# Optimization experiments

Hardware: AMD Instinct MI355X
Metric: run time of the kernel (lower is better)

## Reference

```python
import jax, jax.numpy as jnp
import numpy as np

GF_R = 49      # guided filter radius (hardcoded in module)
GF_EPS = 1.0   # guided filter eps (hardcoded in module)


def edge_pad(x, r):
    # replicate-pad last two dims by r
    return jnp.pad(x, ((0, 0), (0, 0), (r, r), (r, r)), mode='edge')


def boxfilter(x, r):
    # integral-image box filter via cumsum chains, same shape out
    p = edge_pad(x, r)
    c = jnp.cumsum(p, axis=3)
    d = c[:, :, :, 2 * r:] - c[:, :, :, :-2 * r]
    c2 = jnp.cumsum(d, axis=2)
    return c2[:, :, 2 * r:, :] - c2[:, :, :-2 * r, :]


def guided_filter(x, r=GF_R, eps=GF_EPS):
    N = boxfilter(jnp.ones_like(x), r)
    mean_x = boxfilter(x, r) / N
    mean_x2 = boxfilter(x * x, r) / N
    var_x = mean_x2 - mean_x * mean_x   # cov_xy == var_x in the original code
    A = var_x / (var_x + eps)
    bb = mean_x - A * mean_x
    A = boxfilter(A, r) / N
    bb = boxfilter(bb, r) / N
    return A * x + bb


def setup_inputs() -> dict:
    key = jax.random.key(0)
    ks = jax.random.split(key, 12)
    m, n, r = 2048, 4096, 4
    m3 = len(np.arange(m)[::3])  # 683
    return {
        'b': jax.random.normal(ks[0], (1, 1, m, n), jnp.float32),
        'b_negative': jax.random.normal(ks[1], (1, 1, m3, n), jnp.float32),
        'foreground_b': jax.random.uniform(ks[2], (1, 1, m, n), jnp.float32),
        'hX': jax.random.normal(ks[3], (1, 1, m * r, n), jnp.float32),
        'recon_old': jax.random.normal(ks[4], (1, 1, m, n), jnp.float32),
        'fusion_mask': jax.random.uniform(ks[5], (1, 1, m, n), jnp.float32),
        'b_old': jax.random.normal(ks[6], (1, 1, m, n), jnp.float32),
        'r': r,
        'w': jax.random.normal(ks[7], (m, n), jnp.float32),
        'decay_col': jax.random.normal(ks[8], (1, 1, m3, n), jnp.float32),
        'ww': jax.random.normal(ks[9], (m, n), jnp.float32),
    }


def reference(b, b_negative, foreground_b, hX, recon_old, fusion_mask, b_old, r, w, decay_col, ww):
    m, n = w.shape
    b = b * jax.nn.softplus(w)
    # cumsum over coarse rows then bilinear upsample to (m, n)
    decay = jnp.cumsum(b_negative * jax.nn.softplus(decay_col), axis=-2)
    decay = jax.image.resize(decay, (1, 1, m, n), method='linear')
    b = jnp.cumsum(b, axis=-2)
    b = b + decay * (1.0 - foreground_b)
    b_adpt = b * fusion_mask + b_old * (1.0 - fusion_mask)
    diff = guided_filter(hX[:, :, ::r, :] + b_adpt - recon_old)
    diff_adpt = jnp.clip(jnp.diff(diff, axis=-2, prepend=diff[:, :, 0:1, :]), 0.0, None)
    diff_adpt = diff_adpt * jax.nn.softplus(ww)
    diff_adpt = jnp.cumsum(diff_adpt, axis=-2)
    b_adpt = b_adpt - diff_adpt
    return (b_adpt, diff, diff_adpt, b)
```

## Files before the change

kernel.cpp:

```cpp
#include <hip/hip_runtime.h>
#include <cstdint>
#include <cstddef>

#define MR 2048
#define NC 4096
#define M3 683
#define SEG 64
#define HSEG 32
#define SEGD 22
#define H3D 32
#define VT 64
#define VTILES 32
#define NORM (1.0f/9604.0f)
#define SK(k) ((k)+((k)>>4))

__device__ __forceinline__ float sp(float v){
  return fmaxf(v, 0.0f) + log1pf(expf(-fabsf(v)));
}


__global__ void seg_sum_both(const float* __restrict__ bneg, const float* __restrict__ dcol,
                             const float* __restrict__ b, const float* __restrict__ w,
                             float* __restrict__ TD, float* __restrict__ Pd,
                             float* __restrict__ TB, float* __restrict__ Pb){
  int s = blockIdx.x;
  int j = blockIdx.y*blockDim.x + threadIdx.x;
  if(s < SEGD){
    int i0 = s*H3D, i1 = min(M3, i0+H3D);
    float acc = 0.f;
    int i = i0;
    for(; i+8<=i1; i+=8){
      float bv[8], dv[8];
      #pragma unroll
      for(int t=0;t<8;t++){ bv[t]=bneg[(i+t)*NC+j]; dv[t]=dcol[(i+t)*NC+j]; }
      #pragma unroll
      for(int t=0;t<8;t++){ float x=bv[t]*sp(dv[t]); TD[(i+t)*NC+j]=x; acc+=x; }
    }
    for(; i<i1; i++){ float x=bneg[i*NC+j]*sp(dcol[i*NC+j]); TD[i*NC+j]=x; acc+=x; }
    Pd[s*NC+j] = acc;
  } else {
    int sb = s - SEGD;
    int i0 = sb*HSEG;
    float acc=0.f;
    for(int g=0;g<HSEG;g+=8){
      float bv[8], wv[8];
      #pragma unroll
      for(int t=0;t<8;t++){ int i=i0+g+t; bv[t]=b[i*NC+j]; wv[t]=w[i*NC+j]; }
      #pragma unroll
      for(int t=0;t<8;t++){ int i=i0+g+t; float x=bv[t]*sp(wv[t]); TB[i*NC+j]=x; acc+=x; }
    }
    Pb[sb*NC+j]=acc;
  }
}


__global__ void scan_excl_both(float* __restrict__ Pd, float* __restrict__ Pb){
  int j = blockIdx.x*blockDim.x + threadIdx.x;
  {
    float run=0.f; int s=0;
    for(; s+8<=SEGD; s+=8){
      float v[8];
      #pragma unroll
      for(int t=0;t<8;t++) v[t]=Pd[(s+t)*NC+j];
      #pragma unroll
      for(int t=0;t<8;t++){ Pd[(s+t)*NC+j]=run; run+=v[t]; }
    }
    for(; s<SEGD; s++){ float t=Pd[s*NC+j]; Pd[s*NC+j]=run; run+=t; }
  }
  {
    float run=0.f;
    for(int s=0; s<SEG; s+=8){
      float v[8];
      #pragma unroll
      for(int t=0;t<8;t++) v[t]=Pb[(s+t)*NC+j];
      #pragma unroll
      for(int t=0;t<8;t++){ Pb[(s+t)*NC+j]=run; run+=v[t]; }
    }
  }
}

template<int SEGS>
__global__ void scan_excl_t(float* __restrict__ P){
  int j = blockIdx.x*blockDim.x + threadIdx.x;
  float run=0.f;
  int s=0;
  for(; s+8<=SEGS; s+=8){
    float v[8];
    #pragma unroll
    for(int t=0;t<8;t++) v[t]=P[(s+t)*NC+j];
    #pragma unroll
    for(int t=0;t<8;t++){ P[(s+t)*NC+j]=run; run+=v[t]; }
  }
  for(; s<SEGS; s++){ float t=P[s*NC+j]; P[s*NC+j]=run; run+=t; }
}

__global__ void decay_finalize(const float* __restrict__ TD,
                               const float* __restrict__ Pd, float* __restrict__ dc){
  int s=blockIdx.x;
  int j=blockIdx.y*blockDim.x+threadIdx.x;
  int i0=s*H3D, i1=min(M3,i0+H3D);
  float run = Pd[s*NC+j];
  int i=i0;
  for(; i+8<=i1; i+=8){
    float tv[8];
    #pragma unroll
    for(int t=0;t<8;t++) tv[t]=TD[(i+t)*NC+j];
    #pragma unroll
    for(int t=0;t<8;t++){ run+=tv[t]; dc[(i+t)*NC+j]=run; }
  }
  for(; i<i1; i++){ run += TD[i*NC+j]; dc[i*NC+j]=run; }
}

__global__ void phase1(const float* __restrict__ TB,
                       const float* __restrict__ Pb, const float* __restrict__ dc,
                       const float* __restrict__ fg, const float* __restrict__ fm,
                       const float* __restrict__ bold, const float* __restrict__ hX,
                       const float* __restrict__ recon,
                       float* __restrict__ out0, float* __restrict__ out3,
                       float* __restrict__ X){
  int s=blockIdx.x;
  int j=blockIdx.y*blockDim.x+threadIdx.x;
  int i0=s*HSEG;
  float run = Pb[s*NC+j];
  for(int g=0; g<HSEG; g+=8){
    float tb[8], fgv[8], fmv[8], bo[8], hx[8], rc[8], d0[8], d1[8], fw[8];
    #pragma unroll
    for(int t=0;t<8;t++){
      int i=i0+g+t;
      tb[t]=TB[i*NC+j];
      fgv[t]=fg[i*NC+j];
      fmv[t]=fm[i*NC+j];
      bo[t]=bold[i*NC+j];
      hx[t]=hX[(size_t)(4*i)*NC+j];
      rc[t]=recon[i*NC+j];
      float c = (i+0.5f)*(683.0f/2048.0f)-0.5f;
      float fl = floorf(c);
      fw[t] = c-fl;
      int a0=(int)fl, a1=a0+1;
      a0 = a0<0?0:(a0>M3-1?M3-1:a0);
      a1 = a1<0?0:(a1>M3-1?M3-1:a1);
      d0[t]=dc[a0*NC+j]; d1[t]=dc[a1*NC+j];
    }
    #pragma unroll
    for(int t=0;t<8;t++){
      int i=i0+g+t;
      run += tb[t];
      float d = (1.f-fw[t])*d0[t] + fw[t]*d1[t];
      float bf = run + d*(1.f - fgv[t]);
      out3[i*NC+j]=bf;
      float ba = bf*fmv[t] + bo[t]*(1.f-fmv[t]);
      out0[i*NC+j]=ba;
      X[i*NC+j] = hx[t] + ba - rc[t];
    }
  }
}


__global__ __launch_bounds__(256) void hbox_sq(const float* __restrict__ X,
                         float* __restrict__ H1, float* __restrict__ H2){
  __shared__ float C1[SK(NC)+1];
  __shared__ float C2[SK(NC)+1];
  __shared__ float w1[4];
  __shared__ float w2[4];
  int row=blockIdx.x, tid=threadIdx.x;
  int lane = tid & 63, wvid = tid >> 6;
  const float* xr = X + (size_t)row*NC;
  float v1[16], v2[16];
  int base=tid*16;
  float run1=0.f,run2=0.f;
  const float4* p4 = reinterpret_cast<const float4*>(xr+base);
  #pragma unroll
  for(int q=0;q<4;q++){
    float4 fq=p4[q];
    float e[4]={fq.x,fq.y,fq.z,fq.w};
    #pragma unroll
    for(int t=0;t<4;t++){
      run1+=e[t];      v1[q*4+t]=run1;
      run2+=e[t]*e[t]; v2[q*4+t]=run2;
    }
  }
  float s1=run1, s2=run2;
  #pragma unroll
  for(int off=1;off<64;off<<=1){
    float o1=__shfl_up(s1,off);
    float o2=__shfl_up(s2,off);
    if(lane>=off){ s1+=o1; s2+=o2; }
  }
  if(lane==63){ w1[wvid]=s1; w2[wvid]=s2; }
  __syncthreads();
  float b1=0.f,b2=0.f;
  #pragma unroll
  for(int q=0;q<4;q++) if(q<wvid){ b1+=w1[q]; b2+=w2[q]; }
  float ex1 = b1 + s1 - run1, ex2 = b2 + s2 - run2;
  if(tid==0){C1[SK(0)]=0.f;C2[SK(0)]=0.f;}
  #pragma unroll
  for(int e=0;e<16;e++){ int k=base+1+e; C1[SK(k)]=ex1+v1[e]; C2[SK(k)]=ex2+v2[e]; }
  __syncthreads();
  float first1=C1[SK(1)],  last1=C1[SK(NC)]-C1[SK(NC-1)];
  float first2=C2[SK(1)],  last2=C2[SK(NC)]-C2[SK(NC-1)];
  float* h1 = H1+(size_t)row*NC;
  float* h2 = H2+(size_t)row*NC;
  #pragma unroll
  for(int k=0;k<16;k++){
    int j=k*256+tid;
    int lo=j-48, hi=j+49;
    int li = lo<0?0:lo;
    int hc = hi>NC-1?NC-1:hi;
    float s1w=C1[SK(hc+1)]-C1[SK(li)];
    float s2w=C2[SK(hc+1)]-C2[SK(li)];
    if(lo<0){ s1w+=(float)(-lo)*first1; s2w+=(float)(-lo)*first2; }
    if(hi>NC-1){ s1w+=(float)(hi-(NC-1))*last1; s2w+=(float)(hi-(NC-1))*last2; }
    h1[j]=s1w; h2[j]=s2w;
  }
}

__global__ __launch_bounds__(256) void hbox_two(const float* __restrict__ A,
                         const float* __restrict__ B,
                         float* __restrict__ H1, float* __restrict__ H2){
  __shared__ float C1[SK(NC)+1];
  __shared__ float C2[SK(NC)+1];
  __shared__ float w1[4];
  __shared__ float w2[4];
  int row=blockIdx.x, tid=threadIdx.x;
  int lane = tid & 63, wvid = tid >> 6;
  const float* ar = A + (size_t)row*NC;
  const float* br = B + (size_t)row*NC;
  float v1[16], v2[16];
  int base=tid*16;
  float run1=0.f,run2=0.f;
  const float4* pa = reinterpret_cast<const float4*>(ar+base);
  const float4* pb = reinterpret_cast<const float4*>(br+base);
  #pragma unroll
  for(int q=0;q<4;q++){
    float4 fa=pa[q]; float4 fb=pb[q];
    float ea[4]={fa.x,fa.y,fa.z,fa.w};
    float eb[4]={fb.x,fb.y,fb.z,fb.w};
    #pragma unroll
    for(int t=0;t<4;t++){
      run1+=ea[t]; v1[q*4+t]=run1;
      run2+=eb[t]; v2[q*4+t]=run2;
    }
  }
  float s1=run1, s2=run2;
  #pragma unroll
  for(int off=1;off<64;off<<=1){
    float o1=__shfl_up(s1,off);
    float o2=__shfl_up(s2,off);
    if(lane>=off){ s1+=o1; s2+=o2; }
  }
  if(lane==63){ w1[wvid]=s1; w2[wvid]=s2; }
  __syncthreads();
  float b1=0.f,b2=0.f;
  #pragma unroll
  for(int q=0;q<4;q++) if(q<wvid){ b1+=w1[q]; b2+=w2[q]; }
  float ex1 = b1 + s1 - run1, ex2 = b2 + s2 - run2;
  if(tid==0){C1[SK(0)]=0.f;C2[SK(0)]=0.f;}
  #pragma unroll
  for(int e=0;e<16;e++){ int k=base+1+e; C1[SK(k)]=ex1+v1[e]; C2[SK(k)]=ex2+v2[e]; }
  __syncthreads();
  float first1=C1[SK(1)], last1=C1[SK(NC)]-C1[SK(NC-1)];
  float first2=C2[SK(1)], last2=C2[SK(NC)]-C2[SK(NC-1)];
  float* h1 = H1+(size_t)row*NC;
  float* h2 = H2+(size_t)row*NC;
  #pragma unroll
  for(int k=0;k<16;k++){
    int j=k*256+tid;
    int lo=j-48, hi=j+49;
    int li = lo<0?0:lo;
    int hc = hi>NC-1?NC-1:hi;
    float s1w=C1[SK(hc+1)]-C1[SK(li)];
    float s2w=C2[SK(hc+1)]-C2[SK(li)];
    if(lo<0){ s1w+=(float)(-lo)*first1; s2w+=(float)(-lo)*first2; }
    if(hi>NC-1){ s1w+=(float)(hi-(NC-1))*last1; s2w+=(float)(hi-(NC-1))*last2; }
    h1[j]=s1w; h2[j]=s2w;
  }
}


__global__ void vbox_stage1(const float* __restrict__ H1, const float* __restrict__ H2,
                            float* __restrict__ Aimg, float* __restrict__ BBimg){
  int tile = blockIdx.x;
  int j = blockIdx.y*blockDim.x + threadIdx.x;
  int i0 = tile*VT;
  int ip = i0-1;
  float Sa=0.f, Sb=0.f;
  for(int g=0; g<98; g+=14){
    float a1[14], a2[14];
    #pragma unroll
    for(int t=0;t<14;t++){
      int c = ip-48+g+t;
      int cc = c<0?0:(c>MR-1?MR-1:c);
      a1[t]=H1[cc*NC+j]; a2[t]=H2[cc*NC+j];
    }
    #pragma unroll
    for(int t=0;t<14;t++){ Sa+=a1[t]; Sb+=a2[t]; }
  }
  for(int g=0; g<VT; g+=8){
    float hu1[8],hd1[8],hu2[8],hd2[8];
    #pragma unroll
    for(int t=0;t<8;t++){
      int i=i0+g+t;
      int up=i+49; up=up>MR-1?MR-1:up;
      int dn=i-49; dn=dn<0?0:dn;
      hu1[t]=H1[up*NC+j]; hd1[t]=H1[dn*NC+j];
      hu2[t]=H2[up*NC+j]; hd2[t]=H2[dn*NC+j];
    }
    #pragma unroll
    for(int t=0;t<8;t++){
      int i=i0+g+t;
      Sa += hu1[t]-hd1[t];
      Sb += hu2[t]-hd2[t];
      float mx = Sa*NORM, mx2 = Sb*NORM;
      float var = mx2 - mx*mx;
      float A = var/(var+1.0f);
      float bb = mx - A*mx;
      Aimg[i*NC+j]=A; BBimg[i*NC+j]=bb;
    }
  }
}


__global__ void vbox2_fused(const float* __restrict__ H1, const float* __restrict__ H2,
                            const float* __restrict__ X, const float* __restrict__ ww,
                            float* __restrict__ diff, float* __restrict__ S,
                            float* __restrict__ Pc){
  int tile = blockIdx.x;
  int j = blockIdx.y*blockDim.x + threadIdx.x;
  int i0 = tile*VT;
  int ip = i0-1;
  float Sa=0.f, Sb=0.f;
  for(int g=0; g<98; g+=14){
    float a1[14], a2[14];
    #pragma unroll
    for(int t=0;t<14;t++){
      int c = ip-48+g+t;
      int cc = c<0?0:(c>MR-1?MR-1:c);
      a1[t]=H1[cc*NC+j]; a2[t]=H2[cc*NC+j];
    }
    #pragma unroll
    for(int t=0;t<14;t++){ Sa+=a1[t]; Sb+=a2[t]; }
  }
  float dpre, acc=0.f;
  if(tile==0) dpre = 3.0e38f;
  else        dpre = (Sa*NORM)*X[(size_t)ip*NC+j] + Sb*NORM;
  for(int g=0; g<VT; g+=8){
    float hu1[8],hd1[8],hu2[8],hd2[8],xv[8],wv[8];
    #pragma unroll
    for(int t=0;t<8;t++){
      int i=i0+g+t;
      int up=i+49; up=up>MR-1?MR-1:up;
      int dn=i-49; dn=dn<0?0:dn;
      hu1[t]=H1[up*NC+j]; hd1[t]=H1[dn*NC+j];
      hu2[t]=H2[up*NC+j]; hd2[t]=H2[dn*NC+j];
      xv[t]=X[(size_t)i*NC+j]; wv[t]=ww[i*NC+j];
    }
    #pragma unroll
    for(int t=0;t<8;t++){
      int i=i0+g+t;
      Sa += hu1[t]-hd1[t];
      Sb += hu2[t]-hd2[t];
      float d = (Sa*NORM)*xv[t] + Sb*NORM;
      diff[i*NC+j]=d;
      float v = d-dpre; v = v>0.f? v:0.f;
      float sv = v*sp(wv[t]);
      S[i*NC+j]=sv; acc+=sv; dpre=d;
    }
  }
  Pc[tile*NC+j]=acc;
}


__global__ void phase3_final(const float* __restrict__ Pc,
                             float* __restrict__ out0, float* __restrict__ out2){
  int s=blockIdx.x;
  int j=blockIdx.y*blockDim.x+threadIdx.x;
  int i0=s*VT;
  float run = Pc[s*NC+j];
  for(int g=0; g<VT; g+=8){
    float sv[8], o0[8];
    #pragma unroll
    for(int t=0;t<8;t++){ int i=i0+g+t; sv[t]=out2[i*NC+j]; o0[t]=out0[i*NC+j]; }
    #pragma unroll
    for(int t=0;t<8;t++){
      int i=i0+g+t;
      run += sv[t];
      out2[i*NC+j]=run;
      out0[i*NC+j]=o0[t]-run;
    }
  }
}

extern "C" void kernel_launch(void* const* d_in, const int* in_sizes, int n_in,
                              void* d_out, int out_size, void* d_ws, size_t ws_size,
                              hipStream_t stream){
  const float* b    = (const float*)d_in[0];
  const float* bneg = (const float*)d_in[1];
  const float* fg   = (const float*)d_in[2];
  const float* hX   = (const float*)d_in[3];
  const float* recon= (const float*)d_in[4];
  const float* fm   = (const float*)d_in[5];
  const float* bold = (const float*)d_in[6];
  const float* w    = (const float*)d_in[8];
  const float* dcol = (const float*)d_in[9];
  const float* ww   = (const float*)d_in[10];

  float* out  = (float*)d_out;
  float* out0 = out;
  float* out1 = out + (size_t)MR*NC;
  float* out2 = out + 2ull*MR*NC;
  float* out3 = out + 3ull*MR*NC;

  float* wsf = (float*)d_ws;
  float* X  = wsf;
  float* H1 = wsf + 1ull*MR*NC;
  float* H2 = wsf + 2ull*MR*NC;
  float* DC = wsf + 3ull*MR*NC;
  float* Pb = DC + (size_t)M3*NC;
  float* Pd = Pb + (size_t)SEG*NC;
  float* Pc = Pd + (size_t)SEGD*NC;
  float* TD = H1;
  float* TB = H2;

  seg_sum_both <<<dim3(SEGD+SEG,NC/256),256,0,stream>>>(bneg,dcol,b,w,TD,Pd,TB,Pb);
  scan_excl_both<<<NC/256,256,0,stream>>>(Pd,Pb);
  decay_finalize<<<dim3(SEGD,NC/256),256,0,stream>>>(TD,Pd,DC);
  phase1       <<<dim3(SEG, NC/256),256,0,stream>>>(TB,Pb,DC,fg,fm,bold,hX,recon,out0,out3,X);
  hbox_sq      <<<MR,256,0,stream>>>(X,H1,H2);
  vbox_stage1  <<<dim3(VTILES,NC/256),256,0,stream>>>(H1,H2,out1,out2);
  hbox_two     <<<MR,256,0,stream>>>(out1,out2,H1,H2);
  vbox2_fused  <<<dim3(VTILES,NC/256),256,0,stream>>>(H1,H2,X,ww,out1,out2,Pc);
  scan_excl_t<VTILES><<<NC/256,256,0,stream>>>(Pc);
  phase3_final <<<dim3(VTILES,NC/256),256,0,stream>>>(Pc,out0,out2);
}
```

Measured before the change: 569.2 us.

## Vectorize column kernels with float4/float2 accesses and split final scan finer

Column-parallel kernels now handle four (or two) adjacent columns per thread using float4/float2 loads and stores, and the grids shrink to match. The hbox kernels gather each thread's 16 contiguous outputs into registers and write them as float4 stores instead of strided scalar stores. vbox2_fused now emits two partial sums per tile so the final cumulative pass runs over 64 segments, keeping enough blocks in flight. The aim is fewer memory instructions and wider transactions. The cost is higher register pressure and fewer blocks in the wide kernels, which can reduce occupancy.

```diff
diff --git a/kernel.cpp b/kernel.cpp
--- a/kernel.cpp
+++ b/kernel.cpp
@@ -11,8 +11,12 @@
 #define H3D 32
 #define VT 64
 #define VTILES 32
+#define PSEG 64
 #define NORM (1.0f/9604.0f)
 #define SK(k) ((k)+((k)>>4))
+
+union F4u { float4 v; float f[4]; };
+union F2u { float2 v; float f[2]; };
 
 __device__ __forceinline__ float sp(float v){
   return fmaxf(v, 0.0f) + log1pf(expf(-fabsf(v)));
@@ -24,32 +28,52 @@
                              float* __restrict__ TD, float* __restrict__ Pd,
                              float* __restrict__ TB, float* __restrict__ Pb){
   int s = blockIdx.x;
-  int j = blockIdx.y*blockDim.x + threadIdx.x;
+  size_t col = ((size_t)blockIdx.y*blockDim.x + threadIdx.x)*4;
   if(s < SEGD){
     int i0 = s*H3D, i1 = min(M3, i0+H3D);
-    float acc = 0.f;
+    float acc[4]={0.f,0.f,0.f,0.f};
     int i = i0;
     for(; i+8<=i1; i+=8){
-      float bv[8], dv[8];
-      #pragma unroll
-      for(int t=0;t<8;t++){ bv[t]=bneg[(i+t)*NC+j]; dv[t]=dcol[(i+t)*NC+j]; }
-      #pragma unroll
-      for(int t=0;t<8;t++){ float x=bv[t]*sp(dv[t]); TD[(i+t)*NC+j]=x; acc+=x; }
-    }
-    for(; i<i1; i++){ float x=bneg[i*NC+j]*sp(dcol[i*NC+j]); TD[i*NC+j]=x; acc+=x; }
-    Pd[s*NC+j] = acc;
+      F4u bv[8], dv[8];
+      #pragma unroll
+      for(int t=0;t<8;t++){ size_t o=(size_t)(i+t)*NC+col;
+        bv[t].v=*(const float4*)(bneg+o); dv[t].v=*(const float4*)(dcol+o); }
+      #pragma unroll
+      for(int t=0;t<8;t++){
+        F4u x; size_t o=(size_t)(i+t)*NC+col;
+        #pragma unroll
+        for(int k=0;k<4;k++){ x.f[k]=bv[t].f[k]*sp(dv[t].f[k]); acc[k]+=x.f[k]; }
+        *(float4*)(TD+o)=x.v;
+      }
+    }
+    for(; i<i1; i++){
+      F4u bv,dv,x; size_t o=(size_t)i*NC+col;
+      bv.v=*(const float4*)(bneg+o); dv.v=*(const float4*)(dcol+o);
+      #pragma unroll
+      for(int k=0;k<4;k++){ x.f[k]=bv.f[k]*sp(dv.f[k]); acc[k]+=x.f[k]; }
+      *(float4*)(TD+o)=x.v;
+    }
+    F4u a; a.f[0]=acc[0];a.f[1]=acc[1];a.f[2]=acc[2];a.f[3]=acc[3];
+    *(float4*)(Pd+(size_t)s*NC+col)=a.v;
   } else {
     int sb = s - SEGD;
     int i0 = sb*HSEG;
-    float acc=0.f;
+    float acc[4]={0.f,0.f,0.f,0.f};
     for(int g=0;g<HSEG;g+=8){
-      float bv[8], wv[8];
-      #pragma unroll
-      for(int t=0;t<8;t++){ int i=i0+g+t; bv[t]=b[i*NC+j]; wv[t]=w[i*NC+j]; }
-      #pragma unroll
-      for(int t=0;t<8;t++){ int i=i0+g+t; float x=bv[t]*sp(wv[t]); TB[i*NC+j]=x; acc+=x; }
-    }
-    Pb[sb*NC+j]=acc;
+      F4u bv[8], wv[8];
+      #pragma unroll
+      for(int t=0;t<8;t++){ size_t o=(size_t)(i0+g+t)*NC+col;
+        bv[t].v=*(const float4*)(b+o); wv[t].v=*(const float4*)(w+o); }
+      #pragma unroll
+      for(int t=0;t<8;t++){
+        F4u x; size_t o=(size_t)(i0+g+t)*NC+col;
+        #pragma unroll
+        for(int k=0;k<4;k++){ x.f[k]=bv[t].f[k]*sp(wv[t].f[k]); acc[k]+=x.f[k]; }
+        *(float4*)(TB+o)=x.v;
+      }
+    }
+    F4u a; a.f[0]=acc[0];a.f[1]=acc[1];a.f[2]=acc[2];a.f[3]=acc[3];
+    *(float4*)(Pb+(size_t)sb*NC+col)=a.v;
   }
 }
 
@@ -97,18 +121,30 @@
 __global__ void decay_finalize(const float* __restrict__ TD,
                                const float* __restrict__ Pd, float* __restrict__ dc){
   int s=blockIdx.x;
-  int j=blockIdx.y*blockDim.x+threadIdx.x;
+  size_t col = ((size_t)blockIdx.y*blockDim.x + threadIdx.x)*4;
   int i0=s*H3D, i1=min(M3,i0+H3D);
-  float run = Pd[s*NC+j];
+  float run[4];
+  { F4u p; p.v=*(const float4*)(Pd+(size_t)s*NC+col);
+    run[0]=p.f[0];run[1]=p.f[1];run[2]=p.f[2];run[3]=p.f[3]; }
   int i=i0;
   for(; i+8<=i1; i+=8){
-    float tv[8];
-    #pragma unroll
-    for(int t=0;t<8;t++) tv[t]=TD[(i+t)*NC+j];
-    #pragma unroll
-    for(int t=0;t<8;t++){ run+=tv[t]; dc[(i+t)*NC+j]=run; }
-  }
-  for(; i<i1; i++){ run += TD[i*NC+j]; dc[i*NC+j]=run; }
+    F4u tv[8];
+    #pragma unroll
+    for(int t=0;t<8;t++) tv[t].v=*(const float4*)(TD+(size_t)(i+t)*NC+col);
+    #pragma unroll
+    for(int t=0;t<8;t++){
+      F4u o;
+      #pragma unroll
+      for(int k=0;k<4;k++){ run[k]+=tv[t].f[k]; o.f[k]=run[k]; }
+      *(float4*)(dc+(size_t)(i+t)*NC+col)=o.v;
+    }
+  }
+  for(; i<i1; i++){
+    F4u tv,o; tv.v=*(const float4*)(TD+(size_t)i*NC+col);
+    #pragma unroll
+    for(int k=0;k<4;k++){ run[k]+=tv.f[k]; o.f[k]=run[k]; }
+    *(float4*)(dc+(size_t)i*NC+col)=o.v;
+  }
 }
 
 __global__ void phase1(const float* __restrict__ TB,
@@ -119,38 +155,50 @@
                        float* __restrict__ out0, float* __restrict__ out3,
                        float* __restrict__ X){
   int s=blockIdx.x;
-  int j=blockIdx.y*blockDim.x+threadIdx.x;
+  size_t col = ((size_t)blockIdx.y*blockDim.x + threadIdx.x)*4;
   int i0=s*HSEG;
-  float run = Pb[s*NC+j];
-  for(int g=0; g<HSEG; g+=8){
-    float tb[8], fgv[8], fmv[8], bo[8], hx[8], rc[8], d0[8], d1[8], fw[8];
-    #pragma unroll
-    for(int t=0;t<8;t++){
+  float run[4];
+  { F4u p; p.v=*(const float4*)(Pb+(size_t)s*NC+col);
+    run[0]=p.f[0];run[1]=p.f[1];run[2]=p.f[2];run[3]=p.f[3]; }
+  for(int g=0; g<HSEG; g+=4){
+    F4u tb[4], fgv[4], fmv[4], bo[4], hx[4], rc[4], d0[4], d1[4];
+    float fw[4];
+    #pragma unroll
+    for(int t=0;t<4;t++){
       int i=i0+g+t;
-      tb[t]=TB[i*NC+j];
-      fgv[t]=fg[i*NC+j];
-      fmv[t]=fm[i*NC+j];
-      bo[t]=bold[i*NC+j];
-      hx[t]=hX[(size_t)(4*i)*NC+j];
-      rc[t]=recon[i*NC+j];
-      float c = (i+0.5f)*(683.0f/2048.0f)-0.5f;
-      float fl = floorf(c);
-      fw[t] = c-fl;
+      size_t o=(size_t)i*NC+col;
+      tb[t].v =*(const float4*)(TB+o);
+      fgv[t].v=*(const float4*)(fg+o);
+      fmv[t].v=*(const float4*)(fm+o);
+      bo[t].v =*(const float4*)(bold+o);
+      hx[t].v =*(const float4*)(hX+(size_t)(4*i)*NC+col);
+      rc[t].v =*(const float4*)(recon+o);
+      float c=(i+0.5f)*(683.0f/2048.0f)-0.5f;
+      float fl=floorf(c); fw[t]=c-fl;
       int a0=(int)fl, a1=a0+1;
-      a0 = a0<0?0:(a0>M3-1?M3-1:a0);
-      a1 = a1<0?0:(a1>M3-1?M3-1:a1);
-      d0[t]=dc[a0*NC+j]; d1[t]=dc[a1*NC+j];
-    }
-    #pragma unroll
-    for(int t=0;t<8;t++){
+      a0=a0<0?0:(a0>M3-1?M3-1:a0);
+      a1=a1<0?0:(a1>M3-1?M3-1:a1);
+      d0[t].v=*(const float4*)(dc+(size_t)a0*NC+col);
+      d1[t].v=*(const float4*)(dc+(size_t)a1*NC+col);
+    }
+    #pragma unroll
+    for(int t=0;t<4;t++){
       int i=i0+g+t;
-      run += tb[t];
-      float d = (1.f-fw[t])*d0[t] + fw[t]*d1[t];
-      float bf = run + d*(1.f - fgv[t]);
-      out3[i*NC+j]=bf;
-      float ba = bf*fmv[t] + bo[t]*(1.f-fmv[t]);
-      out0[i*NC+j]=ba;
-      X[i*NC+j] = hx[t] + ba - rc[t];
+      size_t o=(size_t)i*NC+col;
+      F4u o3v,o0v,xv;
+      #pragma unroll
+      for(int k=0;k<4;k++){
+        run[k]+=tb[t].f[k];
+        float d=(1.f-fw[t])*d0[t].f[k]+fw[t]*d1[t].f[k];
+        float bf=run[k]+d*(1.f-fgv[t].f[k]);
+        o3v.f[k]=bf;
+        float ba=bf*fmv[t].f[k]+bo[t].f[k]*(1.f-fmv[t].f[k]);
+        o0v.f[k]=ba;
+        xv.f[k]=hx[t].f[k]+ba-rc[t].f[k];
+      }
+      *(float4*)(out3+o)=o3v.v;
+      *(float4*)(out0+o)=o0v.v;
+      *(float4*)(X+o)=xv.v;
     }
   }
 }
@@ -200,9 +248,10 @@
   float first2=C2[SK(1)],  last2=C2[SK(NC)]-C2[SK(NC-1)];
   float* h1 = H1+(size_t)row*NC;
   float* h2 = H2+(size_t)row*NC;
-  #pragma unroll
-  for(int k=0;k<16;k++){
-    int j=k*256+tid;
+  F4u s1o[4], s2o[4];
+  #pragma unroll
+  for(int e=0;e<16;e++){
+    int j=base+e;
     int lo=j-48, hi=j+49;
     int li = lo<0?0:lo;
     int hc = hi>NC-1?NC-1:hi;
@@ -210,7 +259,12 @@
     float s2w=C2[SK(hc+1)]-C2[SK(li)];
     if(lo<0){ s1w+=(float)(-lo)*first1; s2w+=(float)(-lo)*first2; }
     if(hi>NC-1){ s1w+=(float)(hi-(NC-1))*last1; s2w+=(float)(hi-(NC-1))*last2; }
-    h1[j]=s1w; h2[j]=s2w;
+    s1o[e>>2].f[e&3]=s1w; s2o[e>>2].f[e&3]=s2w;
+  }
+  #pragma unroll
+  for(int q=0;q<4;q++){
+    *(float4*)(h1+base+4*q)=s1o[q].v;
+    *(float4*)(h2+base+4*q)=s2o[q].v;
   }
 }
 
@@ -262,9 +316,10 @@
   float first2=C2[SK(1)], last2=C2[SK(NC)]-C2[SK(NC-1)];
   float* h1 = H1+(size_t)row*NC;
   float* h2 = H2+(size_t)row*NC;
-  #pragma unroll
-  for(int k=0;k<16;k++){
-    int j=k*256+tid;
+  F4u s1o[4], s2o[4];
+  #pragma unroll
+  for(int e=0;e<16;e++){
+    int j=base+e;
     int lo=j-48, hi=j+49;
     int li = lo<0?0:lo;
     int hc = hi>NC-1?NC-1:hi;
@@ -272,7 +327,12 @@
     float s2w=C2[SK(hc+1)]-C2[SK(li)];
     if(lo<0){ s1w+=(float)(-lo)*first1; s2w+=(float)(-lo)*first2; }
     if(hi>NC-1){ s1w+=(float)(hi-(NC-1))*last1; s2w+=(float)(hi-(NC-1))*last2; }
-    h1[j]=s1w; h2[j]=s2w;
+    s1o[e>>2].f[e&3]=s1w; s2o[e>>2].f[e&3]=s2w;
+  }
+  #pragma unroll
+  for(int q=0;q<4;q++){
+    *(float4*)(h1+base+4*q)=s1o[q].v;
+    *(float4*)(h2+base+4*q)=s2o[q].v;
   }
 }
 
@@ -280,41 +340,52 @@
 __global__ void vbox_stage1(const float* __restrict__ H1, const float* __restrict__ H2,
                             float* __restrict__ Aimg, float* __restrict__ BBimg){
   int tile = blockIdx.x;
-  int j = blockIdx.y*blockDim.x + threadIdx.x;
+  size_t col = ((size_t)blockIdx.y*blockDim.x + threadIdx.x)*2;
   int i0 = tile*VT;
   int ip = i0-1;
-  float Sa=0.f, Sb=0.f;
+  float Sa[2]={0.f,0.f}, Sb[2]={0.f,0.f};
   for(int g=0; g<98; g+=14){
-    float a1[14], a2[14];
+    F2u a1[14], a2[14];
     #pragma unroll
     for(int t=0;t<14;t++){
       int c = ip-48+g+t;
       int cc = c<0?0:(c>MR-1?MR-1:c);
-      a1[t]=H1[cc*NC+j]; a2[t]=H2[cc*NC+j];
-    }
-    #pragma unroll
-    for(int t=0;t<14;t++){ Sa+=a1[t]; Sb+=a2[t]; }
+      a1[t].v=*(const float2*)(H1+(size_t)cc*NC+col);
+      a2[t].v=*(const float2*)(H2+(size_t)cc*NC+col);
+    }
+    #pragma unroll
+    for(int t=0;t<14;t++){
+      #pragma unroll
+      for(int k=0;k<2;k++){ Sa[k]+=a1[t].f[k]; Sb[k]+=a2[t].f[k]; }
+    }
   }
   for(int g=0; g<VT; g+=8){
-    float hu1[8],hd1[8],hu2[8],hd2[8];
+    F2u hu1[8],hd1[8],hu2[8],hd2[8];
     #pragma unroll
     for(int t=0;t<8;t++){
       int i=i0+g+t;
       int up=i+49; up=up>MR-1?MR-1:up;
       int dn=i-49; dn=dn<0?0:dn;
-      hu1[t]=H1[up*NC+j]; hd1[t]=H1[dn*NC+j];
-      hu2[t]=H2[up*NC+j]; hd2[t]=H2[dn*NC+j];
+      hu1[t].v=*(const float2*)(H1+(size_t)up*NC+col);
+      hd1[t].v=*(const float2*)(H1+(size_t)dn*NC+col);
+      hu2[t].v=*(const float2*)(H2+(size_t)up*NC+col);
+      hd2[t].v=*(const float2*)(H2+(size_t)dn*NC+col);
     }
     #pragma unroll
     for(int t=0;t<8;t++){
       int i=i0+g+t;
-      Sa += hu1[t]-hd1[t];
-      Sb += hu2[t]-hd2[t];
-      float mx = Sa*NORM, mx2 = Sb*NORM;
-      float var = mx2 - mx*mx;
-      float A = var/(var+1.0f);
-      float bb = mx - A*mx;
-      Aimg[i*NC+j]=A; BBimg[i*NC+j]=bb;
+      F2u Av, Bv;
+      #pragma unroll
+      for(int k=0;k<2;k++){
+        Sa[k] += hu1[t].f[k]-hd1[t].f[k];
+        Sb[k] += hu2[t].f[k]-hd2[t].f[k];
+        float mx = Sa[k]*NORM, mx2 = Sb[k]*NORM;
+        float var = mx2 - mx*mx;
+        float A = var/(var+1.0f);
+        Av.f[k]=A; Bv.f[k]=mx - A*mx;
+      }
+      *(float2*)(Aimg+(size_t)i*NC+col)=Av.v;
+      *(float2*)(BBimg+(size_t)i*NC+col)=Bv.v;
     }
   }
 }
@@ -325,67 +396,98 @@
                             float* __restrict__ diff, float* __restrict__ S,
                             float* __restrict__ Pc){
   int tile = blockIdx.x;
-  int j = blockIdx.y*blockDim.x + threadIdx.x;
+  size_t col = ((size_t)blockIdx.y*blockDim.x + threadIdx.x)*2;
   int i0 = tile*VT;
   int ip = i0-1;
-  float Sa=0.f, Sb=0.f;
+  float Sa[2]={0.f,0.f}, Sb[2]={0.f,0.f};
   for(int g=0; g<98; g+=14){
-    float a1[14], a2[14];
+    F2u a1[14], a2[14];
     #pragma unroll
     for(int t=0;t<14;t++){
       int c = ip-48+g+t;
       int cc = c<0?0:(c>MR-1?MR-1:c);
-      a1[t]=H1[cc*NC+j]; a2[t]=H2[cc*NC+j];
-    }
-    #pragma unroll
-    for(int t=0;t<14;t++){ Sa+=a1[t]; Sb+=a2[t]; }
-  }
-  float dpre, acc=0.f;
-  if(tile==0) dpre = 3.0e38f;
-  else        dpre = (Sa*NORM)*X[(size_t)ip*NC+j] + Sb*NORM;
+      a1[t].v=*(const float2*)(H1+(size_t)cc*NC+col);
+      a2[t].v=*(const float2*)(H2+(size_t)cc*NC+col);
+    }
+    #pragma unroll
+    for(int t=0;t<14;t++){
+      #pragma unroll
+      for(int k=0;k<2;k++){ Sa[k]+=a1[t].f[k]; Sb[k]+=a2[t].f[k]; }
+    }
+  }
+  float dpre[2], accA[2]={0.f,0.f}, accB[2]={0.f,0.f};
+  if(tile==0){ dpre[0]=3.0e38f; dpre[1]=3.0e38f; }
+  else {
+    F2u xp; xp.v=*(const float2*)(X+(size_t)ip*NC+col);
+    #pragma unroll
+    for(int k=0;k<2;k++) dpre[k]=(Sa[k]*NORM)*xp.f[k]+Sb[k]*NORM;
+  }
   for(int g=0; g<VT; g+=8){
-    float hu1[8],hd1[8],hu2[8],hd2[8],xv[8],wv[8];
+    F2u hu1[8],hd1[8],hu2[8],hd2[8],xv[8],wv[8];
     #pragma unroll
     for(int t=0;t<8;t++){
       int i=i0+g+t;
       int up=i+49; up=up>MR-1?MR-1:up;
       int dn=i-49; dn=dn<0?0:dn;
-      hu1[t]=H1[up*NC+j]; hd1[t]=H1[dn*NC+j];
-      hu2[t]=H2[up*NC+j]; hd2[t]=H2[dn*NC+j];
-      xv[t]=X[(size_t)i*NC+j]; wv[t]=ww[i*NC+j];
-    }
+      hu1[t].v=*(const float2*)(H1+(size_t)up*NC+col);
+      hd1[t].v=*(const float2*)(H1+(size_t)dn*NC+col);
+      hu2[t].v=*(const float2*)(H2+(size_t)up*NC+col);
+      hd2[t].v=*(const float2*)(H2+(size_t)dn*NC+col);
+      xv[t].v =*(const float2*)(X+(size_t)i*NC+col);
+      wv[t].v =*(const float2*)(ww+(size_t)i*NC+col);
+    }
+    float* acc = (g<VT/2)? accA : accB;
     #pragma unroll
     for(int t=0;t<8;t++){
       int i=i0+g+t;
-      Sa += hu1[t]-hd1[t];
-      Sb += hu2[t]-hd2[t];
-      float d = (Sa*NORM)*xv[t] + Sb*NORM;
-      diff[i*NC+j]=d;
-      float v = d-dpre; v = v>0.f? v:0.f;
-      float sv = v*sp(wv[t]);
-      S[i*NC+j]=sv; acc+=sv; dpre=d;
-    }
-  }
-  Pc[tile*NC+j]=acc;
+      F2u dv, sv;
+      #pragma unroll
+      for(int k=0;k<2;k++){
+        Sa[k] += hu1[t].f[k]-hd1[t].f[k];
+        Sb[k] += hu2[t].f[k]-hd2[t].f[k];
+        float d = (Sa[k]*NORM)*xv[t].f[k] + Sb[k]*NORM;
+        dv.f[k]=d;
+        float v = d-dpre[k]; v = v>0.f? v:0.f;
+        float s = v*sp(wv[t].f[k]);
+        sv.f[k]=s; acc[k]+=s; dpre[k]=d;
+      }
+      *(float2*)(diff+(size_t)i*NC+col)=dv.v;
+      *(float2*)(S+(size_t)i*NC+col)=sv.v;
+    }
+  }
+  F2u pa, pb2;
+  pa.f[0]=accA[0]; pa.f[1]=accA[1];
+  pb2.f[0]=accB[0]; pb2.f[1]=accB[1];
+  *(float2*)(Pc+(size_t)(2*tile)*NC+col)=pa.v;
+  *(float2*)(Pc+(size_t)(2*tile+1)*NC+col)=pb2.v;
 }
 
 
 __global__ void phase3_final(const float* __restrict__ Pc,
                              float* __restrict__ out0, float* __restrict__ out2){
   int s=blockIdx.x;
-  int j=blockIdx.y*blockDim.x+threadIdx.x;
-  int i0=s*VT;
-  float run = Pc[s*NC+j];
-  for(int g=0; g<VT; g+=8){
-    float sv[8], o0[8];
-    #pragma unroll
-    for(int t=0;t<8;t++){ int i=i0+g+t; sv[t]=out2[i*NC+j]; o0[t]=out0[i*NC+j]; }
+  size_t col = ((size_t)blockIdx.y*blockDim.x + threadIdx.x)*4;
+  int i0=s*(MR/PSEG);
+  float run[4];
+  { F4u p; p.v=*(const float4*)(Pc+(size_t)s*NC+col);
+    run[0]=p.f[0];run[1]=p.f[1];run[2]=p.f[2];run[3]=p.f[3]; }
+  for(int g=0; g<MR/PSEG; g+=8){
+    F4u sv[8], o0[8];
+    #pragma unroll
+    for(int t=0;t<8;t++){ size_t o=(size_t)(i0+g+t)*NC+col;
+      sv[t].v=*(const float4*)(out2+o); o0[t].v=*(const float4*)(out0+o); }
     #pragma unroll
     for(int t=0;t<8;t++){
-      int i=i0+g+t;
-      run += sv[t];
-      out2[i*NC+j]=run;
-      out0[i*NC+j]=o0[t]-run;
+      size_t o=(size_t)(i0+g+t)*NC+col;
+      F4u c2, c0;
+      #pragma unroll
+      for(int k=0;k<4;k++){
+        run[k]+=sv[t].f[k];
+        c2.f[k]=run[k];
+        c0.f[k]=o0[t].f[k]-run[k];
+      }
+      *(float4*)(out2+o)=c2.v;
+      *(float4*)(out0+o)=c0.v;
     }
   }
 }
@@ -421,14 +523,14 @@
   float* TD = H1;
   float* TB = H2;
 
-  seg_sum_both <<<dim3(SEGD+SEG,NC/256),256,0,stream>>>(bneg,dcol,b,w,TD,Pd,TB,Pb);
+  seg_sum_both <<<dim3(SEGD+SEG,NC/1024),256,0,stream>>>(bneg,dcol,b,w,TD,Pd,TB,Pb);
   scan_excl_both<<<NC/256,256,0,stream>>>(Pd,Pb);
-  decay_finalize<<<dim3(SEGD,NC/256),256,0,stream>>>(TD,Pd,DC);
-  phase1       <<<dim3(SEG, NC/256),256,0,stream>>>(TB,Pb,DC,fg,fm,bold,hX,recon,out0,out3,X);
+  decay_finalize<<<dim3(SEGD,NC/1024),256,0,stream>>>(TD,Pd,DC);
+  phase1       <<<dim3(SEG, NC/1024),256,0,stream>>>(TB,Pb,DC,fg,fm,bold,hX,recon,out0,out3,X);
   hbox_sq      <<<MR,256,0,stream>>>(X,H1,H2);
-  vbox_stage1  <<<dim3(VTILES,NC/256),256,0,stream>>>(H1,H2,out1,out2);
+  vbox_stage1  <<<dim3(VTILES,NC/512),256,0,stream>>>(H1,H2,out1,out2);
   hbox_two     <<<MR,256,0,stream>>>(out1,out2,H1,H2);
-  vbox2_fused  <<<dim3(VTILES,NC/256),256,0,stream>>>(H1,H2,X,ww,out1,out2,Pc);
-  scan_excl_t<VTILES><<<NC/256,256,0,stream>>>(Pc);
-  phase3_final <<<dim3(VTILES,NC/256),256,0,stream>>>(Pc,out0,out2);
-}
+  vbox2_fused  <<<dim3(VTILES,NC/512),256,0,stream>>>(H1,H2,X,ww,out1,out2,Pc);
+  scan_excl_t<PSEG><<<NC/256,256,0,stream>>>(Pc);
+  phase3_final <<<dim3(PSEG,NC/1024),256,0,stream>>>(Pc,out0,out2);
+}
```

After: 705.5 us. 1.24x slower.
